# Kernel tuning notes

Hardware: AMD Instinct MI355X
Metric: run time of the kernel (lower is better)

## Reference

```python
import jax, jax.numpy as jnp
import numpy as np
from jax import lax

B, L, D, H = 2, 2048, 2048, 16
DH = D // H            # 128 head dim
D_REL = 64             # relevance projection dim (class const)
K = max(1, int(0.25 * L))  # top-K_FRAC tokens per query
NEG_INF = float('-inf')


def setup_inputs() -> dict:
    key = jax.random.key(0)
    ks = jax.random.split(key, 8)
    s = D ** (-0.5)
    return {
        'hidden_states': jax.random.normal(ks[0], (B, L, D), jnp.float32),
        'relevance':     jax.random.normal(ks[1], (B, L, D), jnp.float32),
        # torch nn.Linear weights are [out_features, in_features]
        'W_q_rel': jax.random.normal(ks[2], (D_REL, D), jnp.float32) * s,
        'W_k_rel': jax.random.normal(ks[3], (D_REL, D), jnp.float32) * s,
        'W_q': jax.random.normal(ks[4], (D, D), jnp.float32) * s,
        'W_k': jax.random.normal(ks[5], (D, D), jnp.float32) * s,
        'W_v': jax.random.normal(ks[6], (D, D), jnp.float32) * s,
        'W_o': jax.random.normal(ks[7], (D, D), jnp.float32) * s,
    }


def _rel_scores(relevance, W_q_rel, W_k_rel):
    # low-rank relevance logits, causally masked: [B, L, L]
    q = relevance @ W_q_rel.T   # [B, L, d_rel]
    k = relevance @ W_k_rel.T   # [B, L, d_rel]
    scores = jnp.einsum('bqd,bkd->bqk', q, k) * (D_REL ** -0.5)
    future = jnp.triu(jnp.ones((L, L), dtype=bool), k=1)
    return jnp.where(future[None], NEG_INF, scores)


def _sparse_mask(rel_scores):
    # additive mask [B, 1, L, L]: top-k per query row -> 0.0, else -inf; diag 0.0
    _, topk_idx = lax.top_k(rel_scores, K)            # [B, L, K]
    b = jnp.arange(B)[:, None, None]
    q = jnp.arange(L)[None, :, None]
    mask = jnp.full((B, L, L), NEG_INF, dtype=rel_scores.dtype)
    mask = mask.at[b, q, topk_idx].set(0.0)
    diag = jnp.arange(L)
    mask = mask.at[:, diag, diag].set(0.0)
    return mask[:, None]  # [B, 1, L, L]


def _attention(hidden_states, W_q, W_k, W_v, W_o, add_mask):
    # standard multi-head attention with additive mask (the wrapped frozen attn)
    q = (hidden_states @ W_q.T).reshape(B, L, H, DH)
    k = (hidden_states @ W_k.T).reshape(B, L, H, DH)
    v = (hidden_states @ W_v.T).reshape(B, L, H, DH)
    scores = jnp.einsum('bqhd,bkhd->bhqk', q, k) * (DH ** -0.5)
    scores = scores + add_mask                      # [B, H, L, L]
    p = jax.nn.softmax(scores, axis=-1)
    ctx = jnp.einsum('bhqk,bkhd->bqhd', p, v).reshape(B, L, D)
    return ctx @ W_o.T


def reference(hidden_states, relevance, W_q_rel, W_k_rel, W_q, W_k, W_v, W_o):
    # Phase 1 path (step >= SPARSE_FROM), no external attention_mask:
    # combined = causal(-inf upper-tri) + sparse top-k mask.
    rel = _rel_scores(relevance, W_q_rel, W_k_rel)
    sparse = _sparse_mask(rel)                      # [B, 1, L, L]
    future = jnp.triu(jnp.ones((L, L), dtype=bool), k=1)
    causal = jnp.where(future, NEG_INF, 0.0).astype(hidden_states.dtype)
    combined = causal[None, None] + sparse          # [B, 1, L, L]
    return _attention(hidden_states, W_q, W_k, W_v, W_o, combined)
```

## Files before the change

kernel.cpp:

```cpp
#include <hip/hip_runtime.h>
#include <math.h>
#include <stdint.h>

#define Bb 2
#define Lq 2048
#define Dm 2048
#define Hh 16
#define DH 128
#define DREL 64
#define KTOP 512

#define NEG_INF (-__builtin_huge_valf())

typedef __attribute__((ext_vector_type(8))) short bf16x8;
typedef __attribute__((ext_vector_type(4))) float f32x4;

static __device__ __forceinline__ unsigned short f2bf(float f) {
  unsigned int u = __float_as_uint(f);
  u += 0x7fffu + ((u >> 16) & 1u);
  return (unsigned short)(u >> 16);
}

static __device__ __forceinline__ void gload16(const void* g, void* lds) {
  __builtin_amdgcn_global_load_lds(
      (const __attribute__((address_space(1))) uint32_t*)(uintptr_t)g,
      (__attribute__((address_space(3))) uint32_t*)(uint32_t)(uintptr_t)lds,
      16, 0, 0);
}

__global__ __launch_bounds__(256) void conv_bf16(const float* __restrict__ in,
                                                 unsigned short* __restrict__ out,
                                                 int n8, float scale) {
  const int i = blockIdx.x * 256 + threadIdx.x;
  if (i >= n8) return;
  const float4 f0 = ((const float4*)in)[2 * i];
  const float4 f1 = ((const float4*)in)[2 * i + 1];
  bf16x8 o;
  o[0] = (short)f2bf(f0.x * scale); o[1] = (short)f2bf(f0.y * scale);
  o[2] = (short)f2bf(f0.z * scale); o[3] = (short)f2bf(f0.w * scale);
  o[4] = (short)f2bf(f1.x * scale); o[5] = (short)f2bf(f1.y * scale);
  o[6] = (short)f2bf(f1.z * scale); o[7] = (short)f2bf(f1.w * scale);
  *(bf16x8*)(out + 8 * (size_t)i) = o;
}

__global__ __launch_bounds__(256) void conv_bf16_w4(const float* __restrict__ w0,
                                                    const float* __restrict__ w1,
                                                    const float* __restrict__ w2,
                                                    const float* __restrict__ w3,
                                                    unsigned short* __restrict__ out,
                                                    float s0) {
  const int sel = blockIdx.y;
  const float* in = (sel == 0) ? w0 : (sel == 1) ? w1 : (sel == 2) ? w2 : w3;
  const float scale = (sel == 0) ? s0 : 1.0f;
  const int i = blockIdx.x * 256 + threadIdx.x;
  const float4 f0 = ((const float4*)in)[2 * i];
  const float4 f1 = ((const float4*)in)[2 * i + 1];
  bf16x8 o;
  o[0] = (short)f2bf(f0.x * scale); o[1] = (short)f2bf(f0.y * scale);
  o[2] = (short)f2bf(f0.z * scale); o[3] = (short)f2bf(f0.w * scale);
  o[4] = (short)f2bf(f1.x * scale); o[5] = (short)f2bf(f1.y * scale);
  o[6] = (short)f2bf(f1.z * scale); o[7] = (short)f2bf(f1.w * scale);
  *(bf16x8*)(out + (size_t)sel * Dm * Dm + 8 * (size_t)i) = o;
}

template <bool BF16OUT>
__global__ __launch_bounds__(512, 2) void gemm256(const unsigned short* __restrict__ A,
                                                  const unsigned short* __restrict__ W,
                                                  void* __restrict__ Cv,
                                                  int M, int N, int Kd) {
  __shared__ unsigned short As[2][2][2][128][32];
  __shared__ unsigned short Bs[2][2][2][128][32];

  const int tid = threadIdx.x;
  const int w = tid >> 6;
  const int lane = tid & 63;
  const int l15 = lane & 15;
  const int quad = lane >> 4;
  const int wm = w >> 2;
  const int wn = w & 3;

  const int gy = M >> 8;
  const int nwg = gy * (N >> 8);
  const int cpx = nwg >> 3;
  const int bid = (int)blockIdx.x;
  const int lin = (bid & 7) * cpx + (bid >> 3);
  const int by = lin % gy, bx = lin / gy;
  const int m0 = by * 256, n0 = bx * 256;

  const int srow = w * 16 + (lane >> 2);
  const int sslot = (lane & 3) ^ ((lane >> 3) & 3);
  const unsigned short* aB = A + (size_t)(m0 + srow) * Kd + sslot * 8;
  const unsigned short* bB = W + (size_t)(n0 + srow) * Kd + sslot * 8;
  const size_t hstep = (size_t)128 * Kd;

  f32x4 acc[8][4];
#pragma unroll
  for (int i = 0; i < 8; ++i)
#pragma unroll
    for (int j = 0; j < 4; ++j) acc[i][j] = (f32x4){0.f, 0.f, 0.f, 0.f};

  bf16x8 af[8], bfr[2];
  const int rswz = (quad ^ ((l15 >> 1) & 3)) * 8;

#define ST_A(BUF, S, T)                                                     \
  do {                                                                      \
    const size_t ko = (size_t)(T) * 64 + (S) * 32;                          \
    gload16(aB + ko, &As[BUF][0][S][w * 16][0]);                            \
    gload16(aB + hstep + ko, &As[BUF][1][S][w * 16][0]);                    \
  } while (0)

#define ST_B(BUF, S, T)                                                     \
  do {                                                                      \
    const size_t ko = (size_t)(T) * 64 + (S) * 32;                          \
    gload16(bB + ko, &Bs[BUF][0][S][w * 16][0]);                            \
    gload16(bB + hstep + ko, &Bs[BUF][1][S][w * 16][0]);                    \
  } while (0)

#define LD_A(BUF, S)                                                        \
  _Pragma("unroll") for (int mi = 0; mi < 8; ++mi)                          \
      af[mi] = *(const bf16x8*)&As[BUF][wm][S][mi * 16 + l15][rswz];

#define LD_B(BUF, S, NP)                                                    \
  _Pragma("unroll") for (int ni = 0; ni < 2; ++ni)                          \
      bfr[ni] = *(const bf16x8*)&Bs[BUF][wn >> 1][S]                        \
          [(wn & 1) * 64 + ((NP) * 2 + ni) * 16 + l15][rswz];

#define MFMA16(NP)                                                          \
  do {                                                                      \
    __builtin_amdgcn_s_setprio(1);                                          \
    _Pragma("unroll") for (int mi = 0; mi < 8; ++mi)                        \
        _Pragma("unroll") for (int ni = 0; ni < 2; ++ni)                    \
            acc[mi][(NP) * 2 + ni] = __builtin_amdgcn_mfma_f32_16x16x32_bf16( \
                af[mi], bfr[ni], acc[mi][(NP) * 2 + ni], 0, 0, 0);          \
    __builtin_amdgcn_s_setprio(0);                                          \
  } while (0)

#define SBAR()        asm volatile("s_barrier" ::: "memory")
#define WAITBAR(N)    asm volatile("s_waitcnt vmcnt(" #N ")\ns_barrier" ::: "memory")

  ST_A(0, 0, 0); ST_B(0, 0, 0); ST_A(0, 1, 0); ST_B(0, 1, 0);
  ST_A(1, 0, 1); ST_B(1, 0, 1); ST_A(1, 1, 1);
  WAITBAR(6);

  const int nt = Kd >> 6;
  int buf = 0;
  for (int t = 0; t < nt - 2; ++t) {
    LD_A(buf, 0);
    LD_B(buf, 0, 0);
    ST_B(buf ^ 1, 1, t + 1);
    SBAR();
    MFMA16(0);
    SBAR();
    LD_B(buf, 0, 1);
    ST_A(buf, 0, t + 2);
    WAITBAR(10);
    MFMA16(1);
    SBAR();
    LD_A(buf, 1);
    LD_B(buf, 1, 0);
    ST_B(buf, 0, t + 2);
    SBAR();
    MFMA16(0);
    SBAR();
    LD_B(buf, 1, 1);
    ST_A(buf, 1, t + 2);
    WAITBAR(10);
    MFMA16(1);
    SBAR();
    buf ^= 1;
  }

  ST_B(buf ^ 1, 1, nt - 1);
  WAITBAR(0);
  for (int g = 0; g < 2; ++g) {
    LD_A(buf, 0); LD_B(buf, 0, 0); MFMA16(0);
    LD_B(buf, 0, 1);               MFMA16(1);
    LD_A(buf, 1); LD_B(buf, 1, 0); MFMA16(0);
    LD_B(buf, 1, 1);               MFMA16(1);
    buf ^= 1;
  }
#undef ST_A
#undef ST_B
#undef LD_A
#undef LD_B
#undef MFMA16
#undef SBAR
#undef WAITBAR

#pragma unroll
  for (int im = 0; im < 8; ++im) {
#pragma unroll
    for (int in = 0; in < 4; ++in) {
      const int col = n0 + wn * 64 + in * 16 + l15;
#pragma unroll
      for (int r = 0; r < 4; ++r) {
        const int row = m0 + wm * 128 + im * 16 + quad * 4 + r;
        if (BF16OUT)
          ((unsigned short*)Cv)[(size_t)row * N + col] = f2bf(acc[im][in][r]);
        else
          ((float*)Cv)[(size_t)row * N + col] = acc[im][in][r];
      }
    }
  }
}

#define RKS 8
__global__ __launch_bounds__(256) void relproj2(const float* __restrict__ A,
                                                const float* __restrict__ Wqr,
                                                const float* __restrict__ Wkr,
                                                float* __restrict__ partq,
                                                float* __restrict__ partk, int M) {
  const float* W = blockIdx.z ? Wkr : Wqr;
  float* part = blockIdx.z ? partk : partq;
  __shared__ float As[16][128];
  __shared__ float Bs[16][64];
  const int ks = blockIdx.x;
  const int m0 = blockIdx.y * 128;
  const int tid = threadIdx.x;
  const int tx = tid & 15;
  const int ty = tid >> 4;
  const int lr = tid >> 1, lk = (tid & 1) * 8;
  const int wr = tid >> 2, wk = (tid & 3) * 4;

  float acc[8][4];
#pragma unroll
  for (int i = 0; i < 8; ++i)
#pragma unroll
    for (int j = 0; j < 4; ++j) acc[i][j] = 0.f;

  const int k00 = ks * (Dm / RKS);
  for (int k0 = k00; k0 < k00 + Dm / RKS; k0 += 16) {
    {
      const float* ap = A + (size_t)(m0 + lr) * Dm + k0 + lk;
      float4 a0 = *(const float4*)(ap);
      float4 a1 = *(const float4*)(ap + 4);
      As[lk + 0][lr] = a0.x; As[lk + 1][lr] = a0.y;
      As[lk + 2][lr] = a0.z; As[lk + 3][lr] = a0.w;
      As[lk + 4][lr] = a1.x; As[lk + 5][lr] = a1.y;
      As[lk + 6][lr] = a1.z; As[lk + 7][lr] = a1.w;
    }
    {
      const float* bp = W + (size_t)wr * Dm + k0 + wk;
      float4 b0 = *(const float4*)(bp);
      Bs[wk + 0][wr] = b0.x; Bs[wk + 1][wr] = b0.y;
      Bs[wk + 2][wr] = b0.z; Bs[wk + 3][wr] = b0.w;
    }
    __syncthreads();
#pragma unroll
    for (int kk = 0; kk < 16; ++kk) {
      float af[8], bf[4];
#pragma unroll
      for (int i = 0; i < 8; ++i) af[i] = As[kk][ty * 8 + i];
#pragma unroll
      for (int j = 0; j < 4; ++j) bf[j] = Bs[kk][tx * 4 + j];
#pragma unroll
      for (int i = 0; i < 8; ++i)
#pragma unroll
        for (int j = 0; j < 4; ++j) acc[i][j] += af[i] * bf[j];
    }
    __syncthreads();
  }

#pragma unroll
  for (int i = 0; i < 8; ++i) {
    float* pp = part + ((size_t)ks * M + m0 + ty * 8 + i) * DREL + tx * 4;
    *(float4*)pp = make_float4(acc[i][0], acc[i][1], acc[i][2], acc[i][3]);
  }
}

__global__ __launch_bounds__(256) void relreduce(const float* __restrict__ pq,
                                                 const float* __restrict__ pk,
                                                 float* __restrict__ qrel,
                                                 float* __restrict__ krel, int n4) {
  const int i = blockIdx.x * 256 + threadIdx.x;
  if (i >= n4) return;
  float4 sq = make_float4(0, 0, 0, 0), sk = sq;
  for (int s = 0; s < RKS; ++s) {
    float4 a = ((const float4*)pq)[(size_t)s * n4 + i];
    float4 b = ((const float4*)pk)[(size_t)s * n4 + i];
    sq.x += a.x; sq.y += a.y; sq.z += a.z; sq.w += a.w;
    sk.x += b.x; sk.y += b.y; sk.z += b.z; sk.w += b.w;
  }
  ((float4*)qrel)[i] = sq;
  ((float4*)krel)[i] = sk;
}

__global__ __launch_bounds__(256) void relscore(const float* __restrict__ qrel,
                                                const float* __restrict__ krel,
                                                float* __restrict__ S) {
  const int jt = blockIdx.x, qt = blockIdx.y, b = blockIdx.z;
  if (jt > qt) return;
  __shared__ float As[16][128];
  __shared__ float Bs[16][128];
  const int tid = threadIdx.x;
  const int q0 = qt * 128, j0 = jt * 128;
  const int tx = tid & 15, ty = tid >> 4;
  const int lr = tid >> 1, lk = (tid & 1) * 8;
  const float* Ab = qrel + (size_t)b * Lq * DREL;
  const float* Kb = krel + (size_t)b * Lq * DREL;

  float acc[8][8];
#pragma unroll
  for (int i = 0; i < 8; ++i)
#pragma unroll
    for (int j = 0; j < 8; ++j) acc[i][j] = 0.f;

  for (int k0 = 0; k0 < DREL; k0 += 16) {
    {
      const float* ap = Ab + (size_t)(q0 + lr) * DREL + k0 + lk;
      float4 a0 = *(const float4*)(ap);
      float4 a1 = *(const float4*)(ap + 4);
      As[lk + 0][lr] = a0.x; As[lk + 1][lr] = a0.y;
      As[lk + 2][lr] = a0.z; As[lk + 3][lr] = a0.w;
      As[lk + 4][lr] = a1.x; As[lk + 5][lr] = a1.y;
      As[lk + 6][lr] = a1.z; As[lk + 7][lr] = a1.w;
    }
    {
      const float* bp = Kb + (size_t)(j0 + lr) * DREL + k0 + lk;
      float4 b0 = *(const float4*)(bp);
      float4 b1 = *(const float4*)(bp + 4);
      Bs[lk + 0][lr] = b0.x; Bs[lk + 1][lr] = b0.y;
      Bs[lk + 2][lr] = b0.z; Bs[lk + 3][lr] = b0.w;
      Bs[lk + 4][lr] = b1.x; Bs[lk + 5][lr] = b1.y;
      Bs[lk + 6][lr] = b1.z; Bs[lk + 7][lr] = b1.w;
    }
    __syncthreads();
#pragma unroll
    for (int kk = 0; kk < 16; ++kk) {
      float af[8], bf[8];
#pragma unroll
      for (int i = 0; i < 8; ++i) af[i] = As[kk][ty * 8 + i];
#pragma unroll
      for (int j = 0; j < 8; ++j) bf[j] = Bs[kk][tx * 8 + j];
#pragma unroll
      for (int i = 0; i < 8; ++i)
#pragma unroll
        for (int j = 0; j < 8; ++j) acc[i][j] += af[i] * bf[j];
    }
    __syncthreads();
  }

  const float sc = 0.125f;
#pragma unroll
  for (int i = 0; i < 8; ++i) {
    float* cp = S + ((size_t)b * Lq + q0 + ty * 8 + i) * Lq + j0 + tx * 8;
    ((float4*)cp)[0] = make_float4(acc[i][0] * sc, acc[i][1] * sc, acc[i][2] * sc, acc[i][3] * sc);
    ((float4*)cp)[1] = make_float4(acc[i][4] * sc, acc[i][5] * sc, acc[i][6] * sc, acc[i][7] * sc);
  }
}

__global__ __launch_bounds__(256) void relselect(const float* __restrict__ S,
                                                 uint32_t* __restrict__ mask) {
  const int w = threadIdx.x >> 6;
  const int lane = threadIdx.x & 63;
  const int ridx = blockIdx.x * 4 + w;
  const int qi = ridx & (Lq - 1);
  const int n = qi + 1;
  const float* srow = S + (size_t)ridx * Lq;

  uint32_t keys[32];
#pragma unroll
  for (int t = 0; t < 32; ++t) {
    const int j = t * 64 + lane;
    const uint32_t u = __float_as_uint(srow[j]);
    const uint32_t k = (u & 0x80000000u) ? ~u : (u | 0x80000000u);
    keys[t] = (j < n) ? k : 0u;
  }

  uint32_t kth = 0u;
  if (n > KTOP) {
    uint32_t pref = 0u;
    int rem = KTOP;
    for (int bit = 31; bit >= 0; --bit) {
      const uint32_t cand = pref | (1u << bit);
      const uint32_t lim = 1u << bit;
      int c = 0;
#pragma unroll
      for (int t = 0; t < 32; ++t) c += ((keys[t] ^ cand) < lim) ? 1 : 0;
      c += __shfl_xor(c, 1);
      c += __shfl_xor(c, 2);
      c += __shfl_xor(c, 4);
      c += __shfl_xor(c, 8);
      c += __shfl_xor(c, 16);
      c += __shfl_xor(c, 32);
      if (c >= rem) pref = cand;
      else rem -= c;
    }
    kth = pref;
  }

  uint32_t* mrow = mask + (size_t)ridx * (Lq / 32);
#pragma unroll
  for (int t = 0; t < 32; ++t) {
    const int j = t * 64 + lane;
    const bool ok = (j < n) && (keys[t] >= kth || j == qi);
    const unsigned long long bal = __ballot(ok);
    if (lane == 0) {
      mrow[2 * t] = (uint32_t)bal;
      mrow[2 * t + 1] = (uint32_t)(bal >> 32);
    }
  }
}

#define ATQ 128
#define TK 64
__global__ __launch_bounds__(512, 4) void attn_flash3(const unsigned short* __restrict__ qkv,
                                                      const uint32_t* __restrict__ mask,
                                                      unsigned short* __restrict__ ctx) {
  __shared__ unsigned short Ks[2][TK][136];
  __shared__ unsigned short Vt[2][2][64][72];
  __shared__ uint32_t mw[2][ATQ][2];

  const int qt = (blockIdx.z == 0) ? ((Lq / ATQ) - 1 - (int)blockIdx.x) : (int)blockIdx.x;
  const int h = blockIdx.y;
  const int b = blockIdx.z;
  const int tid = threadIdx.x;
  const int w = tid >> 6;
  const int lane = tid & 63;
  const int l15 = lane & 15;
  const int quad = lane >> 4;
  const int q0 = qt * ATQ;
  const int STR = 3 * Dm;

  const unsigned short* kbp = qkv + 2048;
  const unsigned short* vbp = qkv + 4096;

  const int myq = q0 + w * 16 + l15;
  const unsigned short* qrow = qkv + (size_t)(b * Lq + myq) * STR + h * DH;
  bf16x8 bq[4];
#pragma unroll
  for (int kk = 0; kk < 4; ++kk) bq[kk] = *(const bf16x8*)(qrow + kk * 32 + quad * 8);

  f32x4 O[8];
#pragma unroll
  for (int f = 0; f < 8; ++f) O[f] = (f32x4){0.f, 0.f, 0.f, 0.f};
  float l_lane = 0.f;

  const int nt = (q0 + ATQ) / TK;

  const int skey = (tid & 255) >> 2;
  const int scg  = tid & 3;
  const int mq   = (tid & 255) >> 1;
  const int msel = tid & 1;
  const int tv = tid - 256;
  const int vkp = tv & 31;
  const int vdg = (tv >> 5) & 7;
  const int vhalf = vkp >> 4;
  const int vkp16 = vkp & 15;
  const int dwc = ((vkp16 >> 1) & 3) * 4 + (vkp16 >> 3) * 2 + (vkp16 & 1);

  const uint32_t* mrow_base = mask + (size_t)(b * Lq + q0 + mq) * (Lq / 32) + msel;
  const unsigned short* krow_base = kbp + (size_t)(b * Lq + skey) * STR + h * DH + scg * 32;
  const unsigned short* vrow_base = vbp + (size_t)(b * Lq + 2 * vkp) * STR + h * DH + vdg * 16;

  bf16x8 r0, r1, r2, r3;
  uint32_t mreg = 0;

#define LOADREGS(KT)                                                       \
  do {                                                                     \
    const int kbase_ = (KT) * TK;                                          \
    if (tid < 256) {                                                       \
      const unsigned short* kr = krow_base + (size_t)kbase_ * STR;         \
      r0 = *(const bf16x8*)(kr);                                           \
      r1 = *(const bf16x8*)(kr + 8);                                       \
      r2 = *(const bf16x8*)(kr + 16);                                      \
      r3 = *(const bf16x8*)(kr + 24);                                      \
      mreg = mrow_base[(KT) * 2];                                          \
    } else {                                                               \
      const unsigned short* vr = vrow_base + (size_t)kbase_ * STR;         \
      r0 = *(const bf16x8*)(vr);                                           \
      r1 = *(const bf16x8*)(vr + 8);                                       \
      r2 = *(const bf16x8*)(vr + STR);                                     \
      r3 = *(const bf16x8*)(vr + STR + 8);                                 \
    }                                                                      \
  } while (0)

#define WRITELDS(BUF)                                                      \
  do {                                                                     \
    if (tid < 256) {                                                       \
      *(bf16x8*)&Ks[BUF][skey][scg * 32 + 0]  = r0;                        \
      *(bf16x8*)&Ks[BUF][skey][scg * 32 + 8]  = r1;                        \
      *(bf16x8*)&Ks[BUF][skey][scg * 32 + 16] = r2;                        \
      *(bf16x8*)&Ks[BUF][skey][scg * 32 + 24] = r3;                        \
      mw[BUF][mq][msel] = mreg;                                            \
    } else {                                                               \
      _Pragma("unroll") for (int i = 0; i < 8; ++i) {                      \
        const int d = vdg * 16 + i;                                        \
        const uint32_t pk = (uint32_t)(unsigned short)r0[i] |              \
                            ((uint32_t)(unsigned short)r2[i] << 16);       \
        ((uint32_t*)&Vt[BUF][vhalf][d >> 1][0])[(d & 1) * 16 + dwc] = pk;  \
      }                                                                    \
      _Pragma("unroll") for (int i = 0; i < 8; ++i) {                      \
        const int d = vdg * 16 + 8 + i;                                    \
        const uint32_t pk = (uint32_t)(unsigned short)r1[i] |              \
                            ((uint32_t)(unsigned short)r3[i] << 16);       \
        ((uint32_t*)&Vt[BUF][vhalf][d >> 1][0])[(d & 1) * 16 + dwc] = pk;  \
      }                                                                    \
    }                                                                      \
  } while (0)

  LOADREGS(0);
  WRITELDS(0);
  __syncthreads();

  int buf = 0;
  for (int kt = 0; kt < nt; ++kt) {
    const bool more = (kt + 1 < nt);
    if (more) LOADREGS(kt + 1);

    __builtin_amdgcn_s_setprio(1);
#pragma unroll
    for (int hh = 0; hh < 2; ++hh) {
      f32x4 acc0 = (f32x4){0.f, 0.f, 0.f, 0.f};
      f32x4 acc1 = acc0;
#pragma unroll
      for (int kk = 0; kk < 4; ++kk) {
        bf16x8 a0 = *(const bf16x8*)&Ks[buf][hh * 32 + l15][kk * 32 + quad * 8];
        bf16x8 a1 = *(const bf16x8*)&Ks[buf][hh * 32 + 16 + l15][kk * 32 + quad * 8];
        acc0 = __builtin_amdgcn_mfma_f32_16x16x32_bf16(a0, bq[kk], acc0, 0, 0, 0);
        acc1 = __builtin_amdgcn_mfma_f32_16x16x32_bf16(a1, bq[kk], acc1, 0, 0, 0);
      }

      const uint32_t mword = mw[buf][w * 16 + l15][hh];
      bf16x8 bp;
      float ps = 0.f;
#pragma unroll
      for (int r = 0; r < 4; ++r) {
        const float p0 = ((mword >> (quad * 4 + r)) & 1u) ? __builtin_amdgcn_exp2f(acc0[r]) : 0.f;
        const float p1 = ((mword >> (16 + quad * 4 + r)) & 1u) ? __builtin_amdgcn_exp2f(acc1[r]) : 0.f;
        ps += p0 + p1;
        bp[r] = (short)f2bf(p0);
        bp[4 + r] = (short)f2bf(p1);
      }
      l_lane += ps;

#pragma unroll
      for (int f = 0; f < 8; ++f) {
        const int d = f * 16 + l15;
        bf16x8 av = *(const bf16x8*)&Vt[buf][hh][d >> 1][(d & 1) * 32 + quad * 8];
        O[f] = __builtin_amdgcn_mfma_f32_16x16x32_bf16(av, bp, O[f], 0, 0, 0);
      }
    }
    __builtin_amdgcn_s_setprio(0);

    if (more) WRITELDS(buf ^ 1);
    __syncthreads();
    buf ^= 1;
  }
#undef LOADREGS
#undef WRITELDS

  l_lane += __shfl_xor(l_lane, 16);
  l_lane += __shfl_xor(l_lane, 32);
  const float rl = 1.0f / l_lane;

  unsigned short* orow = ctx + ((size_t)(b * Lq + q0 + w * 16 + l15)) * Dm + h * DH;
#pragma unroll
  for (int f = 0; f < 8; ++f) {
    ushort4 o4;
    o4.x = f2bf(O[f][0] * rl);
    o4.y = f2bf(O[f][1] * rl);
    o4.z = f2bf(O[f][2] * rl);
    o4.w = f2bf(O[f][3] * rl);
    *(ushort4*)(orow + f * 16 + quad * 4) = o4;
  }
}

extern "C" void kernel_launch(void* const* d_in, const int* in_sizes, int n_in,
                              void* d_out, int out_size, void* d_ws, size_t ws_size,
                              hipStream_t stream) {
  const float* hs  = (const float*)d_in[0];
  const float* rel = (const float*)d_in[1];
  const float* Wqr = (const float*)d_in[2];
  const float* Wkr = (const float*)d_in[3];
  const float* Wq  = (const float*)d_in[4];
  const float* Wk  = (const float*)d_in[5];
  const float* Wv  = (const float*)d_in[6];
  const float* Wo  = (const float*)d_in[7];
  float* out = (float*)d_out;

  const int M = Bb * Lq;
  const int ND = Dm * Dm;
  char* ws = (char*)d_ws;
  size_t off = 0;
  float* qrel = (float*)(ws + off); off += (size_t)M * DREL * 4;
  float* krel = (float*)(ws + off); off += (size_t)M * DREL * 4;
  uint32_t* maskb = (uint32_t*)(ws + off); off += (size_t)M * (Lq / 32) * 4;
  float* partq = (float*)(ws + off); off += (size_t)RKS * M * DREL * 4;
  float* partk = (float*)(ws + off); off += (size_t)RKS * M * DREL * 4;
  float* Sbuf = (float*)(ws + off);
  unsigned short* hsb  = (unsigned short*)(ws + off); off += (size_t)M * Dm * 2;
  unsigned short* qkvb = (unsigned short*)(ws + off); off += (size_t)M * 3 * Dm * 2;
  unsigned short* ctxb = (unsigned short*)(ws + off); off += (size_t)M * Dm * 2;
  unsigned short* Wqkvo = (unsigned short*)(ws + off); off += (size_t)4 * ND * 2;

  const dim3 blk(256);
  const int hsN8 = M * Dm / 8;
  const float QSCALE = 0.08838834764831845f * 1.4426950408889634f;

  relproj2<<<dim3(RKS, M / 128, 2), blk, 0, stream>>>(rel, Wqr, Wkr, partq, partk, M);
  relreduce<<<(M * DREL / 4 + 255) / 256, blk, 0, stream>>>(partq, partk, qrel, krel, M * DREL / 4);
  relscore<<<dim3(Lq / 128, Lq / 128, Bb), blk, 0, stream>>>(qrel, krel, Sbuf);
  relselect<<<M / 4, blk, 0, stream>>>(Sbuf, maskb);

  conv_bf16<<<(hsN8 + 255) / 256, blk, 0, stream>>>(hs, hsb, hsN8, 1.0f);
  conv_bf16_w4<<<dim3(ND / 8 / 256, 4), blk, 0, stream>>>(Wq, Wk, Wv, Wo, Wqkvo, QSCALE);

  gemm256<true><<<dim3((M / 256) * (3 * Dm / 256)), dim3(512), 0, stream>>>(
      hsb, Wqkvo, qkvb, M, 3 * Dm, Dm);

  attn_flash3<<<dim3(Lq / ATQ, Hh, Bb), dim3(512), 0, stream>>>(qkvb, maskb, ctxb);

  gemm256<false><<<dim3((M / 256) * (Dm / 256)), dim3(512), 0, stream>>>(
      ctxb, Wqkvo + (size_t)3 * ND, out, M, Dm, Dm);
}
```

Before: 482.7 us.

## Replace 256x256 GEMM with templated 128x256 tile, simpler double-buffered K32 pipeline

The hand-scheduled 256x256 GEMM with its interleaved half-tile prefetch is replaced by a templated kernel that uses 128x256 tiles (MF=4), a K step of 32, and a plain double-buffered loop: prefetch the next K slice, wait, then compute. Launch bounds rise to 4 blocks per CU and the grid doubles, which aims to raise occupancy and fill the CUs better for the QKV and output projections. In exchange, each tile reuses less data, so there is more global and LDS traffic per flop, and the finer-grained MFMA/load interleaving of the old kernel is lost.

```diff
diff --git a/kernel.cpp b/kernel.cpp
--- a/kernel.cpp
+++ b/kernel.cpp
@@ -63,138 +63,108 @@
   *(bf16x8*)(out + (size_t)sel * Dm * Dm + 8 * (size_t)i) = o;
 }
 
-template <bool BF16OUT>
-__global__ __launch_bounds__(512, 2) void gemm256(const unsigned short* __restrict__ A,
-                                                  const unsigned short* __restrict__ W,
-                                                  void* __restrict__ Cv,
-                                                  int M, int N, int Kd) {
-  __shared__ unsigned short As[2][2][2][128][32];
-  __shared__ unsigned short Bs[2][2][2][128][32];
+template <int MF, bool BF16OUT>
+__global__ __launch_bounds__(512, 4) void gemmP(const unsigned short* __restrict__ A,
+                                                const unsigned short* __restrict__ W,
+                                                void* __restrict__ Cv,
+                                                int M, int N, int Kd) {
+  constexpr int BM = MF * 32;
+  __shared__ unsigned short As[2][BM][32];
+  __shared__ unsigned short Bs[2][256][32];
 
   const int tid = threadIdx.x;
+  const int lane = tid & 63;
   const int w = tid >> 6;
-  const int lane = tid & 63;
   const int l15 = lane & 15;
   const int quad = lane >> 4;
   const int wm = w >> 2;
   const int wn = w & 3;
 
-  const int gy = M >> 8;
+  const int gy = M / BM;
   const int nwg = gy * (N >> 8);
   const int cpx = nwg >> 3;
   const int bid = (int)blockIdx.x;
   const int lin = (bid & 7) * cpx + (bid >> 3);
   const int by = lin % gy, bx = lin / gy;
-  const int m0 = by * 256, n0 = bx * 256;
-
-  const int srow = w * 16 + (lane >> 2);
-  const int sslot = (lane & 3) ^ ((lane >> 3) & 3);
+  const int m0 = by * BM, n0 = bx * 256;
+
+  const int srow = tid >> 2;
+  const int sslot = (tid & 3) ^ ((tid >> 3) & 3);
   const unsigned short* aB = A + (size_t)(m0 + srow) * Kd + sslot * 8;
   const unsigned short* bB = W + (size_t)(n0 + srow) * Kd + sslot * 8;
   const size_t hstep = (size_t)128 * Kd;
 
-  f32x4 acc[8][4];
-#pragma unroll
-  for (int i = 0; i < 8; ++i)
+  f32x4 acc[MF][4];
+#pragma unroll
+  for (int i = 0; i < MF; ++i)
 #pragma unroll
     for (int j = 0; j < 4; ++j) acc[i][j] = (f32x4){0.f, 0.f, 0.f, 0.f};
 
-  bf16x8 af[8], bfr[2];
+  bf16x8 af[MF], bfr[2];
   const int rswz = (quad ^ ((l15 >> 1) & 3)) * 8;
 
-#define ST_A(BUF, S, T)                                                     \
+#define ST(BUF, T)                                                          \
   do {                                                                      \
-    const size_t ko = (size_t)(T) * 64 + (S) * 32;                          \
-    gload16(aB + ko, &As[BUF][0][S][w * 16][0]);                            \
-    gload16(aB + hstep + ko, &As[BUF][1][S][w * 16][0]);                    \
+    const size_t ko = (size_t)(T) * 32;                                     \
+    gload16(aB + ko, &As[BUF][w * 16][0]);                                  \
+    if constexpr (MF == 8) gload16(aB + hstep + ko, &As[BUF][(MF == 8 ? 128 : 0) + w * 16][0]); \
+    gload16(bB + ko, &Bs[BUF][w * 16][0]);                                  \
+    gload16(bB + hstep + ko, &Bs[BUF][128 + w * 16][0]);                    \
   } while (0)
 
-#define ST_B(BUF, S, T)                                                     \
-  do {                                                                      \
-    const size_t ko = (size_t)(T) * 64 + (S) * 32;                          \
-    gload16(bB + ko, &Bs[BUF][0][S][w * 16][0]);                            \
-    gload16(bB + hstep + ko, &Bs[BUF][1][S][w * 16][0]);                    \
-  } while (0)
-
-#define LD_A(BUF, S)                                                        \
-  _Pragma("unroll") for (int mi = 0; mi < 8; ++mi)                          \
-      af[mi] = *(const bf16x8*)&As[BUF][wm][S][mi * 16 + l15][rswz];
-
-#define LD_B(BUF, S, NP)                                                    \
+#define LD_A(BUF)                                                           \
+  _Pragma("unroll") for (int mi = 0; mi < MF; ++mi)                         \
+      af[mi] = *(const bf16x8*)&As[BUF][wm * (BM / 2) + mi * 16 + l15][rswz];
+
+#define LD_B(BUF, NP)                                                       \
   _Pragma("unroll") for (int ni = 0; ni < 2; ++ni)                          \
-      bfr[ni] = *(const bf16x8*)&Bs[BUF][wn >> 1][S]                        \
-          [(wn & 1) * 64 + ((NP) * 2 + ni) * 16 + l15][rswz];
-
-#define MFMA16(NP)                                                          \
+      bfr[ni] = *(const bf16x8*)&Bs[BUF][wn * 64 + ((NP) * 2 + ni) * 16 + l15][rswz];
+
+#define MFMA_NP(NP)                                                         \
   do {                                                                      \
     __builtin_amdgcn_s_setprio(1);                                          \
-    _Pragma("unroll") for (int mi = 0; mi < 8; ++mi)                        \
+    _Pragma("unroll") for (int mi = 0; mi < MF; ++mi)                       \
         _Pragma("unroll") for (int ni = 0; ni < 2; ++ni)                    \
             acc[mi][(NP) * 2 + ni] = __builtin_amdgcn_mfma_f32_16x16x32_bf16( \
                 af[mi], bfr[ni], acc[mi][(NP) * 2 + ni], 0, 0, 0);          \
     __builtin_amdgcn_s_setprio(0);                                          \
   } while (0)
 
-#define SBAR()        asm volatile("s_barrier" ::: "memory")
-#define WAITBAR(N)    asm volatile("s_waitcnt vmcnt(" #N ")\ns_barrier" ::: "memory")
-
-  ST_A(0, 0, 0); ST_B(0, 0, 0); ST_A(0, 1, 0); ST_B(0, 1, 0);
-  ST_A(1, 0, 1); ST_B(1, 0, 1); ST_A(1, 1, 1);
-  WAITBAR(6);
-
-  const int nt = Kd >> 6;
+  ST(0, 0);
+
+  const int nt = Kd >> 5;
   int buf = 0;
-  for (int t = 0; t < nt - 2; ++t) {
-    LD_A(buf, 0);
-    LD_B(buf, 0, 0);
-    ST_B(buf ^ 1, 1, t + 1);
-    SBAR();
-    MFMA16(0);
-    SBAR();
-    LD_B(buf, 0, 1);
-    ST_A(buf, 0, t + 2);
-    WAITBAR(10);
-    MFMA16(1);
-    SBAR();
-    LD_A(buf, 1);
-    LD_B(buf, 1, 0);
-    ST_B(buf, 0, t + 2);
-    SBAR();
-    MFMA16(0);
-    SBAR();
-    LD_B(buf, 1, 1);
-    ST_A(buf, 1, t + 2);
-    WAITBAR(10);
-    MFMA16(1);
-    SBAR();
+  for (int t = 0; t < nt; ++t) {
+    if (t + 1 < nt) {
+      ST(buf ^ 1, t + 1);
+      if constexpr (MF == 8)
+        asm volatile("s_waitcnt vmcnt(4)\ns_barrier" ::: "memory");
+      else
+        asm volatile("s_waitcnt vmcnt(3)\ns_barrier" ::: "memory");
+    } else {
+      asm volatile("s_waitcnt vmcnt(0)\ns_barrier" ::: "memory");
+    }
+    LD_A(buf);
+    LD_B(buf, 0);
+    MFMA_NP(0);
+    LD_B(buf, 1);
+    MFMA_NP(1);
+    asm volatile("s_barrier" ::: "memory");
     buf ^= 1;
   }
-
-  ST_B(buf ^ 1, 1, nt - 1);
-  WAITBAR(0);
-  for (int g = 0; g < 2; ++g) {
-    LD_A(buf, 0); LD_B(buf, 0, 0); MFMA16(0);
-    LD_B(buf, 0, 1);               MFMA16(1);
-    LD_A(buf, 1); LD_B(buf, 1, 0); MFMA16(0);
-    LD_B(buf, 1, 1);               MFMA16(1);
-    buf ^= 1;
-  }
-#undef ST_A
-#undef ST_B
+#undef ST
 #undef LD_A
 #undef LD_B
-#undef MFMA16
-#undef SBAR
-#undef WAITBAR
-
-#pragma unroll
-  for (int im = 0; im < 8; ++im) {
+#undef MFMA_NP
+
+#pragma unroll
+  for (int im = 0; im < MF; ++im) {
 #pragma unroll
     for (int in = 0; in < 4; ++in) {
       const int col = n0 + wn * 64 + in * 16 + l15;
 #pragma unroll
       for (int r = 0; r < 4; ++r) {
-        const int row = m0 + wm * 128 + im * 16 + quad * 4 + r;
+        const int row = m0 + wm * (BM / 2) + im * 16 + quad * 4 + r;
         if (BF16OUT)
           ((unsigned short*)Cv)[(size_t)row * N + col] = f2bf(acc[im][in][r]);
         else
@@ -606,11 +576,11 @@
   conv_bf16<<<(hsN8 + 255) / 256, blk, 0, stream>>>(hs, hsb, hsN8, 1.0f);
   conv_bf16_w4<<<dim3(ND / 8 / 256, 4), blk, 0, stream>>>(Wq, Wk, Wv, Wo, Wqkvo, QSCALE);
 
-  gemm256<true><<<dim3((M / 256) * (3 * Dm / 256)), dim3(512), 0, stream>>>(
+  gemmP<4, true><<<dim3((M / 128) * (3 * Dm / 256)), dim3(512), 0, stream>>>(
       hsb, Wqkvo, qkvb, M, 3 * Dm, Dm);
 
   attn_flash3<<<dim3(Lq / ATQ, Hh, Bb), dim3(512), 0, stream>>>(qkvb, maskb, ctxb);
 
-  gemm256<false><<<dim3((M / 256) * (Dm / 256)), dim3(512), 0, stream>>>(
+  gemmP<4, false><<<dim3((M / 128) * (Dm / 256)), dim3(512), 0, stream>>>(
       ctxb, Wqkvo + (size_t)3 * ND, out, M, Dm, Dm);
 }
```

After: 475.4 us. About the same (-1.5%).
